# Performance work log

Hardware: AMD Instinct MI355X
Metric: run time of the kernel (lower is better)

Reference implementation:

```python
import jax, jax.numpy as jnp
import numpy as np

V_DIM, L_DIM, EMBED, HEADS = 1024, 768, 1024, 16
HEAD_DIM = EMBED // HEADS
SCALE = HEADS ** (-0.5)  # faithful to source: num_heads**-0.5
B, NV, NL = 4, 4096, 256


def _xavier(key, shape):
    fan_in, fan_out = shape[0], shape[1]
    lim = (6.0 / (fan_in + fan_out)) ** 0.5
    return jax.random.uniform(key, shape, jnp.float32, -lim, lim)


def setup_inputs() -> dict:
    key = jax.random.key(0)
    ks = jax.random.split(key, 12)
    inp = {
        'v': jax.random.normal(ks[0], (B, NV, V_DIM), jnp.float32),
        'l': jax.random.normal(ks[1], (B, NL, L_DIM), jnp.float32),
        'attention_mask_l': jnp.ones((B, NL), jnp.int32),
        # weights stored as [in, out] so x @ W
        'W_v2q': _xavier(ks[2], (V_DIM, EMBED)), 'b_v2q': jnp.zeros((EMBED,), jnp.float32),
        'W_l2k': _xavier(ks[3], (L_DIM, EMBED)), 'b_l2k': jnp.zeros((EMBED,), jnp.float32),
        'W_v2v': _xavier(ks[4], (V_DIM, EMBED)), 'b_v2v': jnp.zeros((EMBED,), jnp.float32),
        'W_l2v': _xavier(ks[5], (L_DIM, EMBED)), 'b_l2v': jnp.zeros((EMBED,), jnp.float32),
        'W_v2out': _xavier(ks[6], (EMBED, V_DIM)), 'b_v2out': jnp.zeros((V_DIM,), jnp.float32),
        'W_l2out': _xavier(ks[7], (EMBED, L_DIM)), 'b_l2out': jnp.zeros((L_DIM,), jnp.float32),
    }
    return inp


def _heads(x):
    # [B, N, E] -> [B, H, N, D]
    Bx, N, _ = x.shape
    return x.reshape(Bx, N, HEADS, HEAD_DIM).transpose(0, 2, 1, 3)


def reference(v, l, attention_mask_l, W_v2q, b_v2q, W_l2k, b_l2k, W_v2v, b_v2v,
              W_l2v, b_l2v, W_v2out, b_v2out, W_l2out, b_l2out):
    q = _heads(v @ W_v2q + b_v2q)          # [B,H,Nv,D] vision queries
    k = _heads(l @ W_l2k + b_l2k)          # [B,H,Nl,D] language keys
    val_v = _heads(v @ W_v2v + b_v2v)      # [B,H,Nv,D]
    val_l = _heads(l @ W_l2v + b_l2v)      # [B,H,Nl,D]

    # shared score matrix, reused for both softmax directions
    attn = jnp.einsum('bhqd,bhkd->bhqk', q, k) * SCALE  # [B,H,Nv,Nl]

    # vision attends language: mask invalid language tokens
    mask_bias = jnp.where(attention_mask_l[:, None, None, :] == 0, -1e9, 0.0).astype(attn.dtype)
    attn_v = jax.nn.softmax(attn + mask_bias, axis=-1)   # over Nl
    # language attends vision: softmax over vision axis of the same scores
    attn_l = jax.nn.softmax(attn, axis=-2)               # over Nv

    out_v = jnp.einsum('bhqk,bhkd->bhqd', attn_v, val_l)  # [B,H,Nv,D]
    out_l = jnp.einsum('bhqk,bhqd->bhkd', attn_l, val_v)  # [B,H,Nl,D]

    Bx = v.shape[0]
    out_v = out_v.transpose(0, 2, 1, 3).reshape(Bx, -1, EMBED) @ W_v2out + b_v2out
    out_l = out_l.transpose(0, 2, 1, 3).reshape(Bx, -1, EMBED) @ W_l2out + b_l2out
    return out_v, out_l
```

## Files before the change

kernel.cpp:

```cpp
#include <hip/hip_runtime.h>
#include <hip/hip_bf16.h>

#define EMBED 1024
#define HEADS 16
#define HD 64
#define NVTOK 4096
#define NLTOK 256
#define BATCH 4
#define QSCALE 0.25f

typedef __hip_bfloat16 bf16;
typedef __attribute__((ext_vector_type(8))) short bf16x8;
typedef __attribute__((ext_vector_type(4))) float floatx4;

#define MFMA(a, b, c) __builtin_amdgcn_mfma_f32_16x16x32_bf16((a), (b), (c), 0, 0, 0)

static __device__ __forceinline__ short f2bs(float x) {
  bf16 h = __float2bfloat16(x);
  return *reinterpret_cast<short*>(&h);
}
static __device__ __forceinline__ float b2f(bf16 x) { return __bfloat162float(x); }

typedef const __attribute__((address_space(1))) char ga_char;
typedef __attribute__((address_space(3))) char ls_char;
static __device__ __forceinline__ void load_lds16(const void* g, void* lds) {
  __builtin_amdgcn_global_load_lds((ga_char*)g, (ls_char*)(unsigned)(size_t)(lds), 16, 0, 0);
}

__global__ void detect_dtype(const unsigned* __restrict__ v, int* __restrict__ flag) {
  __shared__ int cnt;
  if (threadIdx.x == 0) cnt = 0;
  __syncthreads();
  unsigned u = v[threadIdx.x];
  int mid = (int)((u >> 7) & 0xFF);
  if (mid >= 110 && mid <= 140) atomicAdd(&cnt, 1);
  __syncthreads();
  if (threadIdx.x == 0) {
    flag[0] = (cnt < 192) ? 1 : 0;
    flag[1] = 0;
  }
}

__global__ void convert_to_bf16_v4(const void* __restrict__ src, bf16* __restrict__ dst,
                                   int n4, const int* __restrict__ flag) {
  int i = blockIdx.x * 256 + threadIdx.x;
  if (i >= n4) return;
  short4 o;
  if (flag[0]) {
    float4 f = ((const float4*)src)[i];
    o.x = f2bs(f.x); o.y = f2bs(f.y); o.z = f2bs(f.z); o.w = f2bs(f.w);
  } else {
    o = ((const short4*)src)[i];
  }
  ((short4*)dst)[i] = o;
}

struct WTArgs {
  const void* src[6];
  bf16* dst[6];
  int R[6];
  int C[6];
  float scale[6];
};
__global__ __launch_bounds__(256) void convert_transpose_all(WTArgs a, const int* __restrict__ flag) {
  __shared__ float tile[32][33];
  const int z = blockIdx.y;
  const int R = a.R[z], C = a.C[z];
  const float sc = a.scale[z];
  const int tpc = C >> 5;
  const int nt = (R >> 5) * tpc;
  const int t = blockIdx.x;
  if (t >= nt) return;
  const int r0 = (t / tpc) << 5, c0 = (t % tpc) << 5;
  {
    const int row = threadIdx.x >> 3, cg = (threadIdx.x & 7) << 2;
    if (flag[0]) {
      float4 f = *(const float4*)((const float*)a.src[z] + (size_t)(r0 + row) * C + c0 + cg);
      tile[row][cg] = f.x * sc; tile[row][cg + 1] = f.y * sc;
      tile[row][cg + 2] = f.z * sc; tile[row][cg + 3] = f.w * sc;
    } else {
      short4 f = *(const short4*)((const short*)a.src[z] + (size_t)(r0 + row) * C + c0 + cg);
      tile[row][cg]     = b2f(*(const bf16*)&f.x) * sc;
      tile[row][cg + 1] = b2f(*(const bf16*)&f.y) * sc;
      tile[row][cg + 2] = b2f(*(const bf16*)&f.z) * sc;
      tile[row][cg + 3] = b2f(*(const bf16*)&f.w) * sc;
    }
  }
  __syncthreads();
  {
    const int col = threadIdx.x >> 3, rg = (threadIdx.x & 7) << 2;
    short4 o;
    o.x = f2bs(tile[rg + 0][col]);
    o.y = f2bs(tile[rg + 1][col]);
    o.z = f2bs(tile[rg + 2][col]);
    o.w = f2bs(tile[rg + 3][col]);
    *(short4*)((short*)a.dst[z] + (size_t)(c0 + col) * R + r0 + rg) = o;
  }
}

struct BArgs {
  const void* src[6];
  bf16* dst[6];
  int n[6];
  float scale[6];
};
__global__ void convert_bias_all(BArgs a, const int* __restrict__ flag) {
  int z = blockIdx.y;
  int i = blockIdx.x * 256 + threadIdx.x;
  if (i >= a.n[z]) return;
  float x = flag[0] ? ((const float*)a.src[z])[i] : b2f(((const bf16*)a.src[z])[i]);
  a.dst[z][i] = __float2bfloat16(x * a.scale[z]);
}

__global__ __launch_bounds__(256) void transpose_vl_heads(const bf16* __restrict__ kv,
                                                          bf16* __restrict__ vlT) {
  __shared__ short t[64][72];
  const int bh = blockIdx.y, b = bh >> 4, h = bh & 15;
  const int nl0 = blockIdx.x << 6;
  const int tid = threadIdx.x;
  {
    const int nl = tid >> 2, dg = (tid & 3) << 4;
    const short* s = (const short*)kv + ((size_t)b * NLTOK + nl0 + nl) * 2048 + 1024 + h * HD + dg;
    *(bf16x8*)&t[nl][dg]     = *(const bf16x8*)s;
    *(bf16x8*)&t[nl][dg + 8] = *(const bf16x8*)(s + 8);
  }
  __syncthreads();
  {
    const int d = tid >> 2, ng = (tid & 3) << 4;
    short* o = (short*)vlT + ((size_t)bh * HD + d) * NLTOK + nl0 + ng;
    short tmp[16];
#pragma unroll
    for (int j = 0; j < 16; j++) tmp[j] = t[ng + j][d];
    *(bf16x8*)o       = *(bf16x8*)&tmp[0];
    *(bf16x8*)(o + 8) = *(bf16x8*)&tmp[8];
  }
}

__global__ __launch_bounds__(256) void gemm_nt(
    const bf16* __restrict__ A, const bf16* __restrict__ Bt,
    const bf16* __restrict__ bias, void* __restrict__ Cout, long long coff,
    int M, int N, int K, float alpha, const int* __restrict__ outf) {
  __shared__ short lds_all[16896];
  short* As = lds_all;
  short* Bs = lds_all + 8192;
  const int f32o = outf[0];
  const int tid = threadIdx.x;
  const int wave = tid >> 6, lane = tid & 63;
  const int bm = blockIdx.x * 128, bn = blockIdx.y * 128;
  const int wr = (wave & 1) * 64, wc = (wave >> 1) * 64;
  const int rl = lane & 15, kg = (lane >> 4) * 8;

  const int srow = wave * 16 + (lane >> 2);
  const int scol = (lane & 3) * 8;
  const short* Ag = (const short*)A + (size_t)(bm + srow) * K + scol;
  const short* Bg = (const short*)Bt + (size_t)(bn + srow) * K + scol;
  short* As0l = &As[wave * 512];
  short* As1l = &As[2048 + wave * 512];
  short* As0h = &As[4096 + wave * 512];
  short* As1h = &As[6144 + wave * 512];
  short* Bs0l = &Bs[wave * 512];
  short* Bs1l = &Bs[2048 + wave * 512];
  short* Bs0h = &Bs[4096 + wave * 512];
  short* Bs1h = &Bs[6144 + wave * 512];
  const size_t rstep = (size_t)64 * K;

  floatx4 acc[4][4];
#pragma unroll
  for (int i = 0; i < 4; i++)
#pragma unroll
    for (int j = 0; j < 4; j++) acc[i][j] = (floatx4){0.f, 0.f, 0.f, 0.f};

  for (int k0 = 0; k0 < K; k0 += 64) {
    __syncthreads();
    load_lds16(Ag + k0, As0l);
    load_lds16(Ag + rstep + k0, As1l);
    load_lds16(Ag + k0 + 32, As0h);
    load_lds16(Ag + rstep + k0 + 32, As1h);
    load_lds16(Bg + k0, Bs0l);
    load_lds16(Bg + rstep + k0, Bs1l);
    load_lds16(Bg + k0 + 32, Bs0h);
    load_lds16(Bg + rstep + k0 + 32, Bs1h);
    __syncthreads();
#pragma unroll
    for (int half = 0; half < 2; half++) {
      const short* Ah = &As[half * 4096];
      const short* Bh = &Bs[half * 4096];
      bf16x8 af[4], bfr[4];
#pragma unroll
      for (int i = 0; i < 4; i++) af[i]  = *(const bf16x8*)&Ah[(wr + i * 16 + rl) * 32 + kg];
#pragma unroll
      for (int j = 0; j < 4; j++) bfr[j] = *(const bf16x8*)&Bh[(wc + j * 16 + rl) * 32 + kg];
#pragma unroll
      for (int i = 0; i < 4; i++)
#pragma unroll
        for (int j = 0; j < 4; j++) acc[i][j] = MFMA(af[i], bfr[j], acc[i][j]);
    }
  }

  const int rg = (lane >> 4) * 4;
  __syncthreads();

  if (!f32o) {
#pragma unroll
    for (int j = 0; j < 4; j++) {
      float bv = b2f(bias[bn + wc + j * 16 + rl]);
#pragma unroll
      for (int i = 0; i < 4; i++)
#pragma unroll
        for (int r = 0; r < 4; r++)
          lds_all[(wr + i * 16 + rg + r) * 132 + wc + j * 16 + rl] =
              f2bs((acc[i][j][r] + bv) * alpha);
    }
    __syncthreads();
#pragma unroll
    for (int it = 0; it < 8; it++) {
      int idx = it * 256 + tid;
      int row = idx >> 4, c = idx & 15;
      bf16x8 o = *(const bf16x8*)&lds_all[row * 132 + c * 8];
      *(bf16x8*)((short*)Cout + coff + (long long)(bm + row) * N + bn + c * 8) = o;
    }
  } else {
    float* Cf = (float*)lds_all;
#pragma unroll
    for (int p = 0; p < 2; p++) {
      if ((wave & 1) == p) {
#pragma unroll
        for (int j = 0; j < 4; j++) {
          float bv = b2f(bias[bn + wc + j * 16 + rl]);
#pragma unroll
          for (int i = 0; i < 4; i++)
#pragma unroll
            for (int r = 0; r < 4; r++)
              Cf[(i * 16 + rg + r) * 132 + wc + j * 16 + rl] = (acc[i][j][r] + bv) * alpha;
        }
      }
      __syncthreads();
#pragma unroll
      for (int it = 0; it < 8; it++) {
        int idx = it * 256 + tid;
        int row = idx >> 5, c = idx & 31;
        float4 o = *(const float4*)&Cf[row * 132 + c * 4];
        *(float4*)((float*)Cout + coff + (long long)(bm + p * 64 + row) * N + bn + c * 4) = o;
      }
      if (p == 0) __syncthreads();
    }
  }
}

__global__ __launch_bounds__(256, 3) void attn_fwd_v(
    const bf16* __restrict__ qv,
    const bf16* __restrict__ kv,
    const bf16* __restrict__ vlT,
    const int* __restrict__ mask,
    bf16* __restrict__ ovh,
    float* __restrict__ sfin) {
  __shared__ short kp_lds[256 * 72];
  __shared__ float stf[1024];
  const int tid = threadIdx.x, wave = tid >> 6, lane = tid & 63;
  const int qt = blockIdx.x, bh = blockIdx.y;
  const int b = bh >> 4, h = bh & 15;
  const size_t qrow0 = (size_t)b * NVTOK + qt * 64;
  const size_t krow0 = (size_t)b * NLTOK;
  const int rl = lane & 15, lg = lane >> 4;

#pragma unroll
  for (int it = 0; it < 8; it++) {
    int vv = it * 256 + tid;
    int nl = vv >> 3, c = vv & 7;
    *(bf16x8*)&kp_lds[nl * 72 + c * 8] =
        *(const bf16x8*)((const short*)kv + (krow0 + nl) * 2048 + h * HD + c * 8);
  }
  kp_lds[tid * 72 + 64] = (short)(mask[b * NLTOK + tid] != 0);
  __syncthreads();

  floatx4 sacc[16];
#pragma unroll
  for (int ct = 0; ct < 16; ct++) sacc[ct] = (floatx4){0.f, 0.f, 0.f, 0.f};
  const short* qrow = (const short*)qv + (qrow0 + wave * 16 + rl) * 2048 + h * HD;
  bf16x8 a0 = *(const bf16x8*)(qrow + lg * 8);
  bf16x8 a1 = *(const bf16x8*)(qrow + 32 + lg * 8);
#pragma unroll
  for (int ct = 0; ct < 16; ct++) {
    bf16x8 b0 = *(const bf16x8*)&kp_lds[(ct * 16 + rl) * 72 + lg * 8];
    bf16x8 b1 = *(const bf16x8*)&kp_lds[(ct * 16 + rl) * 72 + 32 + lg * 8];
    sacc[ct] = MFMA(a0, b0, sacc[ct]);
    sacc[ct] = MFMA(a1, b1, sacc[ct]);
  }

  const short* vbase = (const short*)vlT + ((size_t)bh * 64 + wave * 16) * 256;
  bf16x8 vfr[8];
#pragma unroll
  for (int ks = 0; ks < 8; ks++)
    vfr[ks] = *(const bf16x8*)(vbase + (size_t)rl * 256 + ks * 32 + lg * 8);

#pragma unroll
  for (int ct = 0; ct < 16; ct++) {
    float s = __expf(sacc[ct][0]) + __expf(sacc[ct][1]) +
              __expf(sacc[ct][2]) + __expf(sacc[ct][3]);
    s += __shfl_xor(s, 16);
    s += __shfl_xor(s, 32);
    if (lane < 16) stf[wave * 256 + ct * 16 + lane] = s;
  }

  float mb[16];
#pragma unroll
  for (int ct = 0; ct < 16; ct++)
    mb[ct] = kp_lds[(ct * 16 + rl) * 72 + 64] ? 0.0f : -1e9f;

  float rmax[4] = {-1e30f, -1e30f, -1e30f, -1e30f};
#pragma unroll
  for (int ct = 0; ct < 16; ct++)
#pragma unroll
    for (int r = 0; r < 4; r++) {
      sacc[ct][r] += mb[ct];
      rmax[r] = fmaxf(rmax[r], sacc[ct][r]);
    }
#pragma unroll
  for (int r = 0; r < 4; r++) {
    rmax[r] = fmaxf(rmax[r], __shfl_xor(rmax[r], 1));
    rmax[r] = fmaxf(rmax[r], __shfl_xor(rmax[r], 2));
    rmax[r] = fmaxf(rmax[r], __shfl_xor(rmax[r], 4));
    rmax[r] = fmaxf(rmax[r], __shfl_xor(rmax[r], 8));
  }
  float rsum[4] = {0.f, 0.f, 0.f, 0.f};
#pragma unroll
  for (int ct = 0; ct < 16; ct++)
#pragma unroll
    for (int r = 0; r < 4; r++) {
      sacc[ct][r] = __expf(sacc[ct][r] - rmax[r]);
      rsum[r] += sacc[ct][r];
    }
#pragma unroll
  for (int r = 0; r < 4; r++) {
    rsum[r] += __shfl_xor(rsum[r], 1);
    rsum[r] += __shfl_xor(rsum[r], 2);
    rsum[r] += __shfl_xor(rsum[r], 4);
    rsum[r] += __shfl_xor(rsum[r], 8);
    rsum[r] = 1.0f / fmaxf(rsum[r], 1e-20f);
  }
  __syncthreads();

  {
    float s = stf[tid] + stf[256 + tid] + stf[512 + tid] + stf[768 + tid];
    atomicAdd(&sfin[(size_t)bh * 256 + tid], s);
  }

#pragma unroll
  for (int ct = 0; ct < 16; ct++)
#pragma unroll
    for (int r = 0; r < 4; r++)
      kp_lds[(wave * 16 + lg * 4 + r) * 268 + ct * 16 + rl] = f2bs(sacc[ct][r] * rsum[r]);
  __syncthreads();

  floatx4 oacc[4];
#pragma unroll
  for (int mt = 0; mt < 4; mt++) oacc[mt] = (floatx4){0.f, 0.f, 0.f, 0.f};
#pragma unroll
  for (int ks = 0; ks < 8; ks++) {
#pragma unroll
    for (int mt = 0; mt < 4; mt++) {
      bf16x8 af = *(const bf16x8*)&kp_lds[(mt * 16 + rl) * 268 + ks * 32 + lg * 8];
      oacc[mt] = MFMA(af, vfr[ks], oacc[mt]);
    }
  }
  __syncthreads();

#pragma unroll
  for (int mt = 0; mt < 4; mt++)
#pragma unroll
    for (int r = 0; r < 4; r++)
      kp_lds[(mt * 16 + lg * 4 + r) * 72 + wave * 16 + rl] = f2bs(oacc[mt][r]);
  __syncthreads();

#pragma unroll
  for (int pass = 0; pass < 2; pass++) {
    int idx = pass * 256 + tid;
    int row = idx >> 3, c = idx & 7;
    bf16x8 o = *(const bf16x8*)&kp_lds[row * 72 + c * 8];
    *(bf16x8*)((short*)ovh + (qrow0 + row) * EMBED + h * HD + c * 8) = o;
  }
}

__global__ void zero_f32(float* __restrict__ p, int n) {
  int i = blockIdx.x * 256 + threadIdx.x;
  if (i < n) p[i] = 0.f;
}

__global__ __launch_bounds__(256) void attn_fwd_l(
    const bf16* __restrict__ qv,
    const bf16* __restrict__ kv,
    const float* __restrict__ sf,
    float* __restrict__ olacc) {
  __shared__ short k_lds[256 * 72];
  __shared__ short PT[256 * 40];
  __shared__ short vvT[64 * 40];
  __shared__ float sl[256];
  const int tid = threadIdx.x, wave = tid >> 6, lane = tid & 63;
  const int chunk = blockIdx.x, bh = blockIdx.y;
  const int b = bh >> 4, h = bh & 15;
  const size_t krow0 = (size_t)b * NLTOK;
  const size_t qbase = (size_t)b * NVTOK + chunk * 512;
  const int rl = lane & 15, lg = lane >> 4;

#pragma unroll
  for (int it = 0; it < 8; it++) {
    int vvi = it * 256 + tid;
    int nl = vvi >> 3, c = vvi & 7;
    *(bf16x8*)&k_lds[nl * 72 + c * 8] =
        *(const bf16x8*)((const short*)kv + (krow0 + nl) * 2048 + h * HD + c * 8);
  }
  sl[tid] = 1.0f / fmaxf(sf[(size_t)bh * 256 + tid], 1e-20f);
  __syncthreads();

  floatx4 acc[4][4];
#pragma unroll
  for (int rt = 0; rt < 4; rt++)
#pragma unroll
    for (int dt = 0; dt < 4; dt++) acc[rt][dt] = (floatx4){0.f, 0.f, 0.f, 0.f};

  const int qrt = wave & 1, ctb = (wave >> 1) * 8;
  for (int qs = 0; qs < 16; qs++) {
    const short* qrow = (const short*)qv + (qbase + qs * 32 + qrt * 16 + rl) * 2048 + h * HD;
    bf16x8 a0 = *(const bf16x8*)(qrow + lg * 8);
    bf16x8 a1 = *(const bf16x8*)(qrow + 32 + lg * 8);
    floatx4 s8[8];
#pragma unroll
    for (int i = 0; i < 8; i++) {
      int ct = ctb + i;
      bf16x8 b0 = *(const bf16x8*)&k_lds[(ct * 16 + rl) * 72 + lg * 8];
      bf16x8 b1 = *(const bf16x8*)&k_lds[(ct * 16 + rl) * 72 + 32 + lg * 8];
      floatx4 s = (floatx4){0.f, 0.f, 0.f, 0.f};
      s = MFMA(a0, b0, s);
      s = MFMA(a1, b1, s);
      s8[i] = s;
    }
    __syncthreads();
#pragma unroll
    for (int i = 0; i < 8; i++) {
      int col = (ctb + i) * 16 + rl;
      float linv = sl[col];
#pragma unroll
      for (int r = 0; r < 4; r++)
        PT[col * 40 + qrt * 16 + lg * 4 + r] = f2bs(__expf(s8[i][r]) * linv);
    }
    {
      int qq = tid >> 3, c = tid & 7;
      bf16x8 vvv = *(const bf16x8*)((const short*)qv +
                                    (qbase + qs * 32 + qq) * 2048 + 1024 + h * HD + c * 8);
      const short* vp = (const short*)&vvv;
#pragma unroll
      for (int j = 0; j < 8; j++) vvT[(c * 8 + j) * 40 + qq] = vp[j];
    }
    __syncthreads();
#pragma unroll
    for (int rt = 0; rt < 4; rt++) {
      bf16x8 af = *(const bf16x8*)&PT[(wave * 64 + rt * 16 + rl) * 40 + lg * 8];
#pragma unroll
      for (int dt = 0; dt < 4; dt++) {
        bf16x8 bfr = *(const bf16x8*)&vvT[(dt * 16 + rl) * 40 + lg * 8];
        acc[rt][dt] = MFMA(af, bfr, acc[rt][dt]);
      }
    }
  }
#pragma unroll
  for (int rt = 0; rt < 4; rt++)
#pragma unroll
    for (int dt = 0; dt < 4; dt++)
#pragma unroll
      for (int r = 0; r < 4; r++) {
        int nl = wave * 64 + rt * 16 + lg * 4 + r;
        int d = dt * 16 + rl;
        atomicAdd(&olacc[((size_t)b * NLTOK + nl) * EMBED + h * HD + d], acc[rt][dt][r]);
      }
}

__global__ void finalize_out_l(const float* __restrict__ olacc, bf16* __restrict__ olh) {
  int i = blockIdx.x * 256 + threadIdx.x;
  if (i < 1024 * 1024) olh[i] = __float2bfloat16(olacc[i]);
}

extern "C" void kernel_launch(void* const* d_in, const int* in_sizes, int n_in,
                              void* d_out, int out_size, void* d_ws, size_t ws_size,
                              hipStream_t stream) {
  (void)in_sizes; (void)n_in; (void)out_size; (void)ws_size;
  const void* v_raw = d_in[0];
  const void* l_raw = d_in[1];
  const int*  mask  = (const int*)d_in[2];
  const void* W_v2q = d_in[3];  const void* b_v2q = d_in[4];
  const void* W_l2k = d_in[5];  const void* b_l2k = d_in[6];
  const void* W_v2v = d_in[7];  const void* b_v2v = d_in[8];
  const void* W_l2v = d_in[9];  const void* b_l2v = d_in[10];
  const void* W_v2o = d_in[11]; const void* b_v2o = d_in[12];
  const void* W_l2o = d_in[13]; const void* b_l2o = d_in[14];

  char* ws = (char*)d_ws;
  size_t off = 0;
  auto alloc = [&](size_t bytes) -> void* {
    void* p = ws + off;
    off += (bytes + 255) & ~(size_t)255;
    return p;
  };
  int*  flag   = (int*)alloc(256);
  bf16* vb     = (bf16*)alloc((size_t)16777216 * 2);
  bf16* lb     = (bf16*)alloc((size_t)786432 * 2);
  bf16* b_qv   = (bf16*)alloc(4096);
  bf16* b_kvl  = (bf16*)alloc(4096);
  bf16* bov    = (bf16*)alloc(2048);
  bf16* bol    = (bf16*)alloc(1536);
  bf16* Wqv    = (bf16*)alloc((size_t)2048 * 1024 * 2);
  bf16* Wkvl   = (bf16*)alloc((size_t)2048 * 768 * 2);
  bf16* Wt_v2o = (bf16*)alloc((size_t)1024 * 1024 * 2);
  bf16* Wt_l2o = (bf16*)alloc((size_t)768 * 1024 * 2);
  bf16* qvb    = (bf16*)alloc((size_t)16384 * 2048 * 2);
  bf16* kvb    = (bf16*)alloc((size_t)1024 * 2048 * 2);
  bf16* vlT    = (bf16*)alloc((size_t)64 * 64 * 256 * 2);
  float* sfin  = (float*)alloc((size_t)64 * 256 * 4);
  float* olacc = (float*)alloc((size_t)1024 * 1024 * 4);
  bf16* olh    = (bf16*)alloc((size_t)1024 * 1024 * 2);
  bf16* ovh    = vb;

  detect_dtype<<<1, 256, 0, stream>>>((const unsigned*)v_raw, flag);

  convert_to_bf16_v4<<<16384, 256, 0, stream>>>(v_raw, vb, 4194304, flag);
  convert_to_bf16_v4<<<768, 256, 0, stream>>>(l_raw, lb, 196608, flag);

  BArgs ba;
  ba.src[0] = b_v2q; ba.dst[0] = b_qv;         ba.n[0] = 1024; ba.scale[0] = QSCALE;
  ba.src[1] = b_l2k; ba.dst[1] = b_kvl;        ba.n[1] = 1024; ba.scale[1] = 1.0f;
  ba.src[2] = b_v2v; ba.dst[2] = b_qv + 1024;  ba.n[2] = 1024; ba.scale[2] = 1.0f;
  ba.src[3] = b_l2v; ba.dst[3] = b_kvl + 1024; ba.n[3] = 1024; ba.scale[3] = 1.0f;
  ba.src[4] = b_v2o; ba.dst[4] = bov;          ba.n[4] = 1024; ba.scale[4] = 1.0f;
  ba.src[5] = b_l2o; ba.dst[5] = bol;          ba.n[5] = 768;  ba.scale[5] = 1.0f;
  convert_bias_all<<<dim3(4, 6), 256, 0, stream>>>(ba, flag);

  WTArgs wa;
  wa.src[0] = W_v2q; wa.dst[0] = Wqv;                     wa.R[0] = 1024; wa.C[0] = 1024; wa.scale[0] = QSCALE;
  wa.src[1] = W_l2k; wa.dst[1] = Wkvl;                    wa.R[1] = 768;  wa.C[1] = 1024; wa.scale[1] = 1.0f;
  wa.src[2] = W_v2v; wa.dst[2] = Wqv + (size_t)1024*1024; wa.R[2] = 1024; wa.C[2] = 1024; wa.scale[2] = 1.0f;
  wa.src[3] = W_l2v; wa.dst[3] = Wkvl + (size_t)1024*768; wa.R[3] = 768;  wa.C[3] = 1024; wa.scale[3] = 1.0f;
  wa.src[4] = W_v2o; wa.dst[4] = Wt_v2o;                  wa.R[4] = 1024; wa.C[4] = 1024; wa.scale[4] = 1.0f;
  wa.src[5] = W_l2o; wa.dst[5] = Wt_l2o;                  wa.R[5] = 1024; wa.C[5] = 768;  wa.scale[5] = 1.0f;
  convert_transpose_all<<<dim3(1024, 6), 256, 0, stream>>>(wa, flag);

  zero_f32<<<64, 256, 0, stream>>>(sfin, 64 * 256);
  zero_f32<<<4096, 256, 0, stream>>>(olacc, 1024 * 1024);

  const int* bf16out = flag + 1;
  gemm_nt<<<dim3(128, 16), 256, 0, stream>>>(vb, Wqv, b_qv, qvb, 0, 16384, 2048, 1024, 1.0f, bf16out);
  gemm_nt<<<dim3(8, 16), 256, 0, stream>>>(lb, Wkvl, b_kvl, kvb, 0, 1024, 2048, 768, 1.0f, bf16out);
  transpose_vl_heads<<<dim3(4, 64), 256, 0, stream>>>(kvb, vlT);

  attn_fwd_v<<<dim3(64, 64), 256, 0, stream>>>(qvb, kvb, vlT, mask, ovh, sfin);
  attn_fwd_l<<<dim3(8, 64), 256, 0, stream>>>(qvb, kvb, sfin, olacc);
  finalize_out_l<<<4096, 256, 0, stream>>>(olacc, olh);

  gemm_nt<<<dim3(128, 8), 256, 0, stream>>>(ovh, Wt_v2o, bov, d_out, 0, 16384, 1024, 1024, 1.0f, flag);
  gemm_nt<<<dim3(8, 6), 256, 0, stream>>>(olh, Wt_l2o, bol, d_out, 16777216LL, 1024, 768, 1024, 1.0f, flag);
}
```

Measured before the change: 489.2 us.

## Add 256x256-tile double-buffered GEMM for the large vision projections

Adds a new 512-thread GEMM kernel with 256x256 output tiles, double-buffered 128 KB LDS staging via direct global-to-LDS loads, XCD-aware block swizzling, and s_setprio/barrier interleaving around the MFMA phases. It is used for the two large vision-side GEMMs (the fused Q/V projection and the v2out projection). The larger tiles raise arithmetic intensity per global load and reduce tile reloads. In exchange occupancy drops to a couple of blocks per CU, and the grid for the output projection has only 256 blocks, which may leave CUs underused.

```diff
diff --git a/kernel.cpp b/kernel.cpp
--- a/kernel.cpp
+++ b/kernel.cpp
@@ -247,6 +247,195 @@
   }
 }
 
+#define VMCNT8() do { asm volatile("s_waitcnt vmcnt(8)" ::: "memory"); \
+                      __builtin_amdgcn_sched_barrier(0); } while (0)
+#define VMCNT0() do { asm volatile("s_waitcnt vmcnt(0)" ::: "memory"); \
+                      __builtin_amdgcn_sched_barrier(0); } while (0)
+#define P_PRE()  do { __builtin_amdgcn_s_barrier(); \
+                      asm volatile("s_waitcnt lgkmcnt(0)" ::: "memory"); \
+                      __builtin_amdgcn_sched_barrier(0); \
+                      __builtin_amdgcn_s_setprio(1); } while (0)
+#define P_POST() do { __builtin_amdgcn_s_setprio(0); \
+                      __builtin_amdgcn_sched_barrier(0); \
+                      __builtin_amdgcn_s_barrier(); } while (0)
+
+static __device__ __forceinline__ void compute_tile256(
+    const short* __restrict__ Ab, const short* __restrict__ Bb,
+    floatx4 (&acc)[8][4], int wm, int wn, int rl, int lg) {
+  const int sw = rl & 7;
+  bf16x8 a[4][2], b0[2][2], b1[2][2];
+#define LDA256(m, kk) (*(const bf16x8*)&Ab[(wm * 128 + (m) * 16 + rl) * 64 + ((((kk) * 4 + lg) ^ sw) * 8)])
+#define LDB256(n, kk) (*(const bf16x8*)&Bb[(wn * 64 + (n) * 16 + rl) * 64 + ((((kk) * 4 + lg) ^ sw) * 8)])
+#pragma unroll
+  for (int m = 0; m < 4; m++) { a[m][0] = LDA256(m, 0); a[m][1] = LDA256(m, 1); }
+#pragma unroll
+  for (int n = 0; n < 2; n++) { b0[n][0] = LDB256(n, 0); b0[n][1] = LDB256(n, 1); }
+  P_PRE();
+#pragma unroll
+  for (int m = 0; m < 4; m++)
+#pragma unroll
+    for (int n = 0; n < 2; n++) {
+      acc[m][n] = MFMA(a[m][0], b0[n][0], acc[m][n]);
+      acc[m][n] = MFMA(a[m][1], b0[n][1], acc[m][n]);
+    }
+  P_POST();
+#pragma unroll
+  for (int n = 0; n < 2; n++) { b1[n][0] = LDB256(n + 2, 0); b1[n][1] = LDB256(n + 2, 1); }
+  P_PRE();
+#pragma unroll
+  for (int m = 0; m < 4; m++)
+#pragma unroll
+    for (int n = 0; n < 2; n++) {
+      acc[m][n + 2] = MFMA(a[m][0], b1[n][0], acc[m][n + 2]);
+      acc[m][n + 2] = MFMA(a[m][1], b1[n][1], acc[m][n + 2]);
+    }
+  P_POST();
+#pragma unroll
+  for (int m = 0; m < 4; m++) { a[m][0] = LDA256(m + 4, 0); a[m][1] = LDA256(m + 4, 1); }
+  P_PRE();
+#pragma unroll
+  for (int m = 0; m < 4; m++)
+#pragma unroll
+    for (int n = 0; n < 2; n++) {
+      acc[m + 4][n + 2] = MFMA(a[m][0], b1[n][0], acc[m + 4][n + 2]);
+      acc[m + 4][n + 2] = MFMA(a[m][1], b1[n][1], acc[m + 4][n + 2]);
+    }
+  P_POST();
+  P_PRE();
+#pragma unroll
+  for (int m = 0; m < 4; m++)
+#pragma unroll
+    for (int n = 0; n < 2; n++) {
+      acc[m + 4][n] = MFMA(a[m][0], b0[n][0], acc[m + 4][n]);
+      acc[m + 4][n] = MFMA(a[m][1], b0[n][1], acc[m + 4][n]);
+    }
+  P_POST();
+#undef LDA256
+#undef LDB256
+}
+
+__global__ __launch_bounds__(512, 2) void gemm256_nt(
+    const bf16* __restrict__ A, const bf16* __restrict__ Bt,
+    const bf16* __restrict__ bias, void* __restrict__ Cout, long long coff,
+    int M, int N, int K, float alpha, const int* __restrict__ outf) {
+  extern __shared__ short lds[];
+  short* A0 = lds;
+  short* B0 = lds + 16384;
+  short* A1 = lds + 32768;
+  short* B1 = lds + 49152;
+  const int f32o = outf[0];
+  const int tid = threadIdx.x;
+  const int wave = tid >> 6, lane = tid & 63;
+  const int rl = lane & 15, lg = lane >> 4;
+  const int wm = wave >> 2, wn = wave & 3;
+
+  const int nwg = gridDim.x;
+  const int nMT = M >> 8;
+  {
+  }
+  int orig = blockIdx.x;
+  int qq = nwg >> 3, rr = nwg & 7, xcd = orig & 7, sidx = orig >> 3;
+  int swz = (xcd < rr) ? (xcd * (qq + 1) + sidx)
+                       : (rr * (qq + 1) + (xcd - rr) * qq + sidx);
+  const int bm = (swz % nMT) * 256;
+  const int bn = (swz / nMT) * 256;
+
+  const int r8 = lane >> 3;
+  const int cgs = (lane & 7) ^ r8;
+  const short* ga = (const short*)A + (size_t)(bm + wave * 8 + r8) * K + cgs * 8;
+  const short* gb = (const short*)Bt + (size_t)(bn + wave * 8 + r8) * K + cgs * 8;
+
+#define STAGE256(LA, LB, k0_) do {                                          \
+    _Pragma("unroll")                                                       \
+    for (int p = 0; p < 4; p++) {                                           \
+      load_lds16(ga + (size_t)(p * 64) * K + (k0_), (LA) + wave * 512 + p * 4096); \
+      load_lds16(gb + (size_t)(p * 64) * K + (k0_), (LB) + wave * 512 + p * 4096); \
+    }                                                                       \
+  } while (0)
+
+  floatx4 acc[8][4];
+#pragma unroll
+  for (int m = 0; m < 8; m++)
+#pragma unroll
+    for (int n = 0; n < 4; n++) acc[m][n] = (floatx4){0.f, 0.f, 0.f, 0.f};
+
+  const int NT = K >> 6;
+  STAGE256(A0, B0, 0);
+  STAGE256(A1, B1, 64);
+  int kt = 0;
+  for (; kt + 2 < NT; kt += 2) {
+    VMCNT8();
+    __builtin_amdgcn_s_barrier();
+    compute_tile256(A0, B0, acc, wm, wn, rl, lg);
+    STAGE256(A0, B0, (kt + 2) * 64);
+    VMCNT8();
+    __builtin_amdgcn_s_barrier();
+    compute_tile256(A1, B1, acc, wm, wn, rl, lg);
+    STAGE256(A1, B1, (kt + 3) * 64);
+  }
+  VMCNT8();
+  __builtin_amdgcn_s_barrier();
+  compute_tile256(A0, B0, acc, wm, wn, rl, lg);
+  VMCNT0();
+  __builtin_amdgcn_s_barrier();
+  compute_tile256(A1, B1, acc, wm, wn, rl, lg);
+  __syncthreads();
+
+  if (!f32o) {
+#pragma unroll
+    for (int p = 0; p < 2; p++) {
+      if (wm == p) {
+#pragma unroll
+        for (int n = 0; n < 4; n++) {
+          float bv = b2f(bias[bn + wn * 64 + n * 16 + rl]);
+#pragma unroll
+          for (int m = 0; m < 8; m++)
+#pragma unroll
+            for (int r2 = 0; r2 < 4; r2++)
+              lds[(m * 16 + lg * 4 + r2) * 264 + wn * 64 + n * 16 + rl] =
+                  f2bs((acc[m][n][r2] + bv) * alpha);
+        }
+      }
+      __syncthreads();
+#pragma unroll
+      for (int it = 0; it < 8; it++) {
+        int idx2 = it * 512 + tid;
+        int row = idx2 >> 5, c = idx2 & 31;
+        bf16x8 o = *(const bf16x8*)&lds[row * 264 + c * 8];
+        *(bf16x8*)((short*)Cout + coff + (long long)(bm + p * 128 + row) * N + bn + c * 8) = o;
+      }
+      __syncthreads();
+    }
+  } else {
+    float* Cf = (float*)lds;
+#pragma unroll
+    for (int p = 0; p < 4; p++) {
+      if (wm == (p >> 1)) {
+#pragma unroll
+        for (int n = 0; n < 4; n++) {
+          float bv = b2f(bias[bn + wn * 64 + n * 16 + rl]);
+#pragma unroll
+          for (int mm = 0; mm < 4; mm++)
+#pragma unroll
+            for (int r2 = 0; r2 < 4; r2++)
+              Cf[(mm * 16 + lg * 4 + r2) * 260 + wn * 64 + n * 16 + rl] =
+                  (acc[(p & 1) * 4 + mm][n][r2] + bv) * alpha;
+        }
+      }
+      __syncthreads();
+#pragma unroll
+      for (int it = 0; it < 8; it++) {
+        int idx2 = it * 512 + tid;
+        int row = idx2 >> 6, c = idx2 & 63;
+        float4 o = *(const float4*)&Cf[row * 260 + c * 4];
+        *(float4*)((float*)Cout + coff + (long long)(bm + p * 64 + row) * N + bn + c * 4) = o;
+      }
+      __syncthreads();
+    }
+  }
+#undef STAGE256
+}
+
 __global__ __launch_bounds__(256, 3) void attn_fwd_v(
     const bf16* __restrict__ qv,
     const bf16* __restrict__ kv,
@@ -492,6 +681,13 @@
   const void* W_l2v = d_in[9];  const void* b_l2v = d_in[10];
   const void* W_v2o = d_in[11]; const void* b_v2o = d_in[12];
   const void* W_l2o = d_in[13]; const void* b_l2o = d_in[14];
+
+  static bool lds_attr_ok = false;
+  if (!lds_attr_ok) {
+    hipFuncSetAttribute((const void*)gemm256_nt,
+                        hipFuncAttributeMaxDynamicSharedMemorySize, 131072);
+    lds_attr_ok = true;
+  }
 
   char* ws = (char*)d_ws;
   size_t off = 0;
@@ -546,7 +742,7 @@
   zero_f32<<<4096, 256, 0, stream>>>(olacc, 1024 * 1024);
 
   const int* bf16out = flag + 1;
-  gemm_nt<<<dim3(128, 16), 256, 0, stream>>>(vb, Wqv, b_qv, qvb, 0, 16384, 2048, 1024, 1.0f, bf16out);
+  gemm256_nt<<<512, 512, 131072, stream>>>(vb, Wqv, b_qv, qvb, 0, 16384, 2048, 1024, 1.0f, bf16out);
   gemm_nt<<<dim3(8, 16), 256, 0, stream>>>(lb, Wkvl, b_kvl, kvb, 0, 1024, 2048, 768, 1.0f, bf16out);
   transpose_vl_heads<<<dim3(4, 64), 256, 0, stream>>>(kvb, vlT);
 
@@ -554,6 +750,6 @@
   attn_fwd_l<<<dim3(8, 64), 256, 0, stream>>>(qvb, kvb, sfin, olacc);
   finalize_out_l<<<4096, 256, 0, stream>>>(olacc, olh);
 
-  gemm_nt<<<dim3(128, 8), 256, 0, stream>>>(ovh, Wt_v2o, bov, d_out, 0, 16384, 1024, 1024, 1.0f, flag);
+  gemm256_nt<<<256, 512, 131072, stream>>>(ovh, Wt_v2o, bov, d_out, 0, 16384, 1024, 1024, 1.0f, flag);
   gemm_nt<<<dim3(8, 6), 256, 0, stream>>>(olh, Wt_l2o, bol, d_out, 16777216LL, 1024, 768, 1024, 1.0f, flag);
 }
```

Result: slower. 632.0 us (+29.2%).
